# Optimization experiments

Measured on AMD Instinct MI355X. Metric: run time of the kernel, lower is better.

Reference implementation:

```python
import jax, jax.numpy as jnp
import numpy as np

N_VIEW = 100      # hardcoded n_view in _hard_anchor_sampling
TEMP = 20.0       # self.temperature
BASE_TEMP = 0.1   # self.base_temperature


def _sample_one(x, yh, yp, key):
    # x: [N, D] flattened spatial features, yh = labels, yp = predict (flattened)
    N = yh.shape[0]
    ar = jnp.arange(N)
    hard_mask = (yh == 0) & (yp == 0)            # (y_hat==0)&(y==0)
    easy_mask = (yh == 1) & (yp == 1)            # (y_hat==1)&(y==1)
    # torch keeps the first 50 hard nonzero indices (randperm over range(50) only permutes them)
    hard_idx = jnp.argsort(jnp.where(hard_mask, ar, N))[:N_VIEW // 2]
    # torch keeps a random 50-subset of the easy positives (randperm sampling)
    scores = jnp.where(easy_mask, jax.random.uniform(key, (N,)), -1.0)
    _, easy_idx = jax.lax.top_k(scores, N_VIEW // 2)
    # X_[ii, 0:50] = easy, X_[ii, 50:100] = hard
    return jnp.concatenate([x[easy_idx], x[hard_idx]], axis=0)  # [100, D]


def _contrastive(X_):
    # X_: [2, 100, D]; torch.cat(torch.unbind(X_, dim=1), dim=0) interleaves views-major
    A = jnp.swapaxes(X_, 0, 1).reshape(2 * N_VIEW, -1)  # [200, D]
    # F.normalize (contrast_feature is the same normalized anchor in the source)
    A = A / jnp.maximum(jnp.linalg.norm(A, axis=1, keepdims=True), 1e-12)
    logits = (A @ A.T) / BASE_TEMP
    logits = logits - jax.lax.stop_gradient(jnp.max(logits, axis=1, keepdims=True))
    idx = jnp.arange(2 * N_VIEW)
    # mask = kron([[1,0],[0,1]], ones(100,100)) -> 100x100 block diagonal
    mask0 = (idx[:, None] // N_VIEW == idx[None, :] // N_VIEW).astype(logits.dtype)
    neg_mask = 1.0 - mask0  # computed BEFORE logits_mask is applied
    # scatter_(1, arange(100).view(-1,1), 0) on a 200x200 tensor only zeros the
    # diagonal of the first 100 rows
    r = jnp.arange(N_VIEW)
    logits_mask = jnp.ones_like(mask0).at[r, r].set(0.0)
    mask = mask0 * logits_mask
    exp_l = jnp.exp(logits)
    neg = (exp_l * neg_mask).sum(axis=1, keepdims=True)
    log_prob = jnp.log(exp_l / (exp_l + neg))
    mean_lpp = (log_prob * mask).sum(axis=1) / mask.sum(axis=1)
    return -(mean_lpp / TEMP).mean()


def _forward(feats, labels, predict):
    B, D = feats.shape[0], feats.shape[1]
    x = jnp.moveaxis(feats, 1, -1).reshape(B, -1, D)  # [B, N, D]
    yh = labels.reshape(B, -1)
    yp = predict.reshape(B, -1)
    keys = jax.random.split(jax.random.key(42), B)
    X_ = jax.vmap(_sample_one)(x, yh, yp, keys)       # [2, 100, D]
    return _contrastive(X_)


def setup_inputs() -> dict:
    key = jax.random.key(0)
    k1, k2, k3 = jax.random.split(key, 3)
    feats = jax.random.normal(k1, (2, 128, 32, 64, 64), dtype=jnp.float32)
    labels = jax.random.randint(k2, (2, 32, 64, 64), 0, 2)
    predict = jax.random.randint(k3, (2, 32, 64, 64), 0, 2)
    return {"feats": feats, "labels": labels, "predict": predict}


def reference(feats, labels, predict):
    return _forward(feats, labels, predict)
```

## Files before the change

### kernel.cpp

```cpp
#include <hip/hip_runtime.h>
#include <stdint.h>

#define NPIX   131072
#define HALFN  65536
#define KSEL   50
#define CAP_E  1024
#define CAP_H  2048
#define THR    0.99f
#define CSTR   32
#define SENT_HARD 0xFFFFFFFFu
#define SENT_NONE 0xFFFFFFFEu

__host__ __device__ __forceinline__ uint32_t rotl32(uint32_t v, int d) {
  return (v << d) | (v >> (32 - d));
}

__host__ __device__ __forceinline__ void tf_block(uint32_t k0, uint32_t k1,
                                                  uint32_t c0, uint32_t c1,
                                                  uint32_t& o0, uint32_t& o1) {
  uint32_t ks2 = k0 ^ k1 ^ 0x1BD11BDAu;
  uint32_t x0 = c0 + k0, x1 = c1 + k1;
#define TF_R(r) { x0 += x1; x1 = rotl32(x1, (r)); x1 ^= x0; }
  TF_R(13) TF_R(15) TF_R(26) TF_R(6)   x0 += k1;  x1 += ks2 + 1u;
  TF_R(17) TF_R(29) TF_R(16) TF_R(24)  x0 += ks2; x1 += k0  + 2u;
  TF_R(13) TF_R(15) TF_R(26) TF_R(6)   x0 += k0;  x1 += k1  + 3u;
  TF_R(17) TF_R(29) TF_R(16) TF_R(24)  x0 += k1;  x1 += ks2 + 4u;
  TF_R(13) TF_R(15) TF_R(26) TF_R(6)   x0 += ks2; x1 += k0  + 5u;
#undef TF_R
  o0 = x0; o1 = x1;
}

__global__ void k_zero(int* cnts, float* out) {
  int i = threadIdx.x;
  if (i < 8 * CSTR) cnts[i] = 0;
  if (i == 0) out[0] = 0.f;
}

__global__ __launch_bounds__(512) void k_scores(
    const int* __restrict__ labels, const int* __restrict__ predict,
    uint32_t* __restrict__ scores, uint64_t* __restrict__ ecand,
    uint32_t* __restrict__ hcand, int* __restrict__ cnts,
    uint32_t k00, uint32_t k01, uint32_t k10, uint32_t k11) {
  int gid = blockIdx.x * blockDim.x + threadIdx.x;
  int b = gid >> 17;
  int n = gid & (NPIX - 1);
  int tid = threadIdx.x, wv = tid >> 6, lane = tid & 63;
  int yh = labels[gid], yp = predict[gid];
  bool is_easy = (yh == 1 && yp == 1);
  bool is_hard = (yh == 0 && yp == 0);
  uint32_t sval = SENT_NONE;
  float u = -1.f;
  if (is_easy) {
    uint32_t ka = b ? k10 : k00, kb = b ? k11 : k01;
    uint32_t o0, o1, bits;
    if (n < HALFN) { tf_block(ka, kb, (uint32_t)n, (uint32_t)(n + HALFN), o0, o1); bits = o0; }
    else           { tf_block(ka, kb, (uint32_t)(n - HALFN), (uint32_t)n, o0, o1); bits = o1; }
    u = __uint_as_float((bits >> 9) | 0x3F800000u) - 1.0f;
    sval = __float_as_uint(u);
  } else if (is_hard) {
    sval = SENT_HARD;
  }
  scores[gid] = sval;

  bool cand_e = is_easy && (u >= THR);
  bool cand_h = is_hard && (n < CAP_H);
  uint64_t bal_e  = __ballot(is_easy), bal_h  = __ballot(is_hard);
  uint64_t bal_ec = __ballot(cand_e),  bal_hc = __ballot(cand_h);

  __shared__ int we[8], wh[8], wec[8], whc[8];
  __shared__ int base_ec, base_hc;
  if (lane == 0) {
    we[wv]  = __popcll(bal_e);  wh[wv]  = __popcll(bal_h);
    wec[wv] = __popcll(bal_ec); whc[wv] = __popcll(bal_hc);
  }
  __syncthreads();
  if (tid == 0) {
    int te = 0, th = 0, tec = 0, thc = 0;
    for (int w = 0; w < 8; ++w) { te += we[w]; th += wh[w]; tec += wec[w]; thc += whc[w]; }
    if (te) atomicAdd(&cnts[(b * 4 + 0) * CSTR], te);
    if (th) atomicAdd(&cnts[(b * 4 + 2) * CSTR], th);
    base_ec = tec ? atomicAdd(&cnts[(b * 4 + 1) * CSTR], tec) : 0;
    base_hc = thc ? atomicAdd(&cnts[(b * 4 + 3) * CSTR], thc) : 0;
  }
  __syncthreads();
  if (cand_e) {
    int pre = 0;
    for (int w = 0; w < wv; ++w) pre += wec[w];
    int p = base_ec + pre + __popcll(bal_ec & ((1ull << lane) - 1));
    if (p < CAP_E)
      ecand[b * CAP_E + p] = ((uint64_t)sval << 32) | (uint32_t)(~(uint32_t)n);
  }
  if (cand_h) {
    int pre = 0;
    for (int w = 0; w < wv; ++w) pre += whc[w];
    int p = base_hc + pre + __popcll(bal_hc & ((1ull << lane) - 1));
    hcand[b * CAP_H + p] = (uint32_t)n;
  }
}

__device__ __forceinline__ bool cond_eval(uint32_t s, int cid) {
  return cid == 0 ? (s >= SENT_NONE) : (cid == 1 ? (s == SENT_HARD) : (s != SENT_HARD));
}

__device__ int nth_min_pred(const uint32_t* __restrict__ sc, int want, int cid,
                            int tid, int lane, int wv, uint32_t* s_w32, int* foundcnt) {
  int prev = -1;
  int k = 0;
  for (; k <= want; ++k) {
    uint32_t lmin = 0xFFFFFFFFu;
    for (int m = tid; m < NPIX; m += 128) {
      if (cond_eval(sc[m], cid) && m > prev && (uint32_t)m < lmin) lmin = (uint32_t)m;
    }
    for (int off = 32; off; off >>= 1) {
      uint32_t o = (uint32_t)__shfl_down(lmin, off);
      if (o < lmin) lmin = o;
    }
    if (lane == 0) s_w32[wv] = lmin;
    __syncthreads();
    uint32_t g = s_w32[0] < s_w32[1] ? s_w32[0] : s_w32[1];
    __syncthreads();
    if (g == 0xFFFFFFFFu) break;
    prev = (int)g;
  }
  *foundcnt = k;
  return prev;
}

__global__ __launch_bounds__(128) void k_selgather(
    const uint32_t* __restrict__ scores, const uint64_t* __restrict__ ecand,
    const uint32_t* __restrict__ hcand, const int* __restrict__ cnts,
    const float* __restrict__ feats, float* __restrict__ A) {
  int r = blockIdx.x;
  int tid = threadIdx.x;
  int lane = tid & 63, wv = tid >> 6;
  int v = r & 1, i = r >> 1;
  int b = v;
  const uint32_t* sc = scores + (size_t)b * NPIX;

  __shared__ uint64_t se[CAP_E];
  __shared__ uint32_t shd[CAP_H];
  __shared__ uint32_t s_w32[2];
  __shared__ uint64_t s_w64[2];
  __shared__ int s_n;

  int et = cnts[(b * 4 + 0) * CSTR], ec = cnts[(b * 4 + 1) * CSTR];
  int ht = cnts[(b * 4 + 2) * CSTR], hc = cnts[(b * 4 + 3) * CSTR];

  if (i < KSEL) {
    int eneed = et < KSEL ? et : KSEL;
    bool fast = (ec <= CAP_E) && (ec >= eneed);
    if (fast) {
      int take = ec < KSEL ? ec : KSEL;
      if (i < take) {
        for (int t = tid; t < ec; t += 128) se[t] = ecand[b * CAP_E + t];
        __syncthreads();
        for (int t = tid; t < ec; t += 128) {
          uint64_t mine = se[t];
          int rank = 0;
          for (int j = 0; j < ec; ++j) rank += (se[j] > mine);
          if (rank == i) s_n = (int)(~(uint32_t)mine);
        }
        __syncthreads();
      } else {
        int fc;
        int nsel = nth_min_pred(sc, i - take, 0, tid, lane, wv, s_w32, &fc);
        if (tid == 0) s_n = nsel;
        __syncthreads();
      }
    } else {
      uint64_t prev = 0xFFFFFFFFFFFFFFFFull;
      int found = 0, nsel = -1;
      for (int k = 0; k <= i; ++k) {
        uint64_t lmax = 0;
        for (int m = tid; m < NPIX; m += 128) {
          uint32_t s = sc[m];
          if (s < SENT_NONE) {
            uint64_t key = ((uint64_t)s << 32) | (uint32_t)(~(uint32_t)m);
            if (key < prev && key > lmax) lmax = key;
          }
        }
        for (int off = 32; off; off >>= 1) {
          uint64_t o = __shfl_down(lmax, off);
          if (o > lmax) lmax = o;
        }
        if (lane == 0) s_w64[wv] = lmax;
        __syncthreads();
        uint64_t g = s_w64[0] > s_w64[1] ? s_w64[0] : s_w64[1];
        __syncthreads();
        if (g == 0) break;
        prev = g; found = k + 1;
        if (k == i) nsel = (int)(~(uint32_t)g);
      }
      if (nsel < 0) {
        int fc;
        nsel = nth_min_pred(sc, i - found, 0, tid, lane, wv, s_w32, &fc);
      }
      if (tid == 0) s_n = nsel;
      __syncthreads();
    }
  } else {
    int j = i - KSEL;
    int hneed = ht < KSEL ? ht : KSEL;
    bool fast = (hc >= hneed);
    if (fast) {
      int take = hc < KSEL ? hc : KSEL;
      if (j < take) {
        for (int t = tid; t < hc; t += 128) shd[t] = hcand[b * CAP_H + t];
        __syncthreads();
        for (int t = tid; t < hc; t += 128) {
          uint32_t mine = shd[t];
          int rank = 0;
          for (int m = 0; m < hc; ++m) rank += (shd[m] < mine);
          if (rank == j) s_n = (int)mine;
        }
        __syncthreads();
      } else {
        int fc;
        int nsel = nth_min_pred(sc, j - take, 2, tid, lane, wv, s_w32, &fc);
        if (tid == 0) s_n = nsel;
        __syncthreads();
      }
    } else {
      int fc = 0;
      int nsel = nth_min_pred(sc, j, 1, tid, lane, wv, s_w32, &fc);
      if (fc < j + 1) {
        int fc2;
        nsel = nth_min_pred(sc, j - fc, 2, tid, lane, wv, s_w32, &fc2);
      }
      if (tid == 0) s_n = nsel;
      __syncthreads();
    }
  }

  int n = s_n;
  float val = feats[((size_t)(v * 128 + tid)) * NPIX + (size_t)n];
  float sq = val * val;
  for (int off = 32; off; off >>= 1) sq += __shfl_down(sq, off);
  __shared__ float wsum[2];
  __shared__ float s_inv;
  if (lane == 0) wsum[wv] = sq;
  __syncthreads();
  if (tid == 0) s_inv = 1.0f / fmaxf(sqrtf(wsum[0] + wsum[1]), 1e-12f);
  __syncthreads();
  A[r * 128 + tid] = val * s_inv;
}

__global__ __launch_bounds__(256) void k_loss(const float* __restrict__ A,
                                              float* __restrict__ out) {
  int r = blockIdx.x;
  int c = threadIdx.x;
  __shared__ float arow[128];
  __shared__ float red[256];
  if (c < 128) arow[c] = A[r * 128 + c];
  __syncthreads();
  bool valid = c < 200;
  float logit = -1e30f;
  if (valid) {
    const float* Ac = A + c * 128;
    float dot = 0.f;
#pragma unroll 8
    for (int d = 0; d < 128; ++d) dot += arow[d] * Ac[d];
    logit = dot * 10.0f;
  }
  red[c] = logit;
  __syncthreads();
  for (int s = 128; s; s >>= 1) { if (c < s) { float o = red[c + s]; if (o > red[c]) red[c] = o; } __syncthreads(); }
  float M = red[0];
  __syncthreads();
  float e = valid ? expf(logit - M) : 0.f;
  bool sameblk = valid && ((r / 100) == (c / 100));
  red[c] = (valid && !sameblk) ? e : 0.f;
  __syncthreads();
  for (int s = 128; s; s >>= 1) { if (c < s) red[c] += red[c + s]; __syncthreads(); }
  float neg = red[0];
  __syncthreads();
  bool msk = sameblk && !(r < 100 && c == r);
  red[c] = msk ? ((logit - M) - logf(e + neg)) : 0.f;
  __syncthreads();
  for (int s = 128; s; s >>= 1) { if (c < s) red[c] += red[c + s]; __syncthreads(); }
  if (c == 0) {
    float denom = (r < 100) ? 99.f : 100.f;
    atomicAdd(out, -(red[0] / denom) / (20.0f * 200.0f));
  }
}

extern "C" void kernel_launch(void* const* d_in, const int* in_sizes, int n_in,
                              void* d_out, int out_size, void* d_ws, size_t ws_size,
                              hipStream_t stream) {
  const float* feats  = (const float*)d_in[0];
  const int* labels   = (const int*)d_in[1];
  const int* predict  = (const int*)d_in[2];
  float* out = (float*)d_out;

  char* ws = (char*)d_ws;
  uint32_t* scores = (uint32_t*)ws;
  uint64_t* ecand  = (uint64_t*)(ws + (size_t)2 * NPIX * 4);
  uint32_t* hcand  = (uint32_t*)((char*)ecand + 2 * CAP_E * 8);
  int* cnts  = (int*)((char*)hcand + 2 * CAP_H * 4);
  float* A   = (float*)(cnts + 8 * CSTR);

  uint32_t a0, a1, b0, b1;
  tf_block(0u, 42u, 0u, 2u, a0, a1);
  tf_block(0u, 42u, 1u, 3u, b0, b1);

  k_zero<<<1, 256, 0, stream>>>(cnts, out);
  k_scores<<<(2 * NPIX) / 512, 512, 0, stream>>>(labels, predict, scores, ecand, hcand, cnts, a0, b0, a1, b1);
  k_selgather<<<200, 128, 0, stream>>>(scores, ecand, hcand, cnts, feats, A);
  k_loss<<<200, 256, 0, stream>>>(A, out);
}
```

Baseline: 202.5 us.

## Fuse all four kernels into one cooperative kernel with grid syncs

```diff
diff --git a/kernel.cpp b/kernel.cpp
--- a/kernel.cpp
+++ b/kernel.cpp
@@ -1,5 +1,8 @@
 #include <hip/hip_runtime.h>
+#include <hip/hip_cooperative_groups.h>
 #include <stdint.h>
+
+namespace cg = cooperative_groups;
 
 #define NPIX   131072
 #define HALFN  65536
@@ -10,6 +13,9 @@
 #define CSTR   32
 #define SENT_HARD 0xFFFFFFFFu
 #define SENT_NONE 0xFFFFFFFEu
+#define NBLK   256
+#define NTHR   512
+#define NWAVE  (NTHR / 64)
 
 __host__ __device__ __forceinline__ uint32_t rotl32(uint32_t v, int d) {
   return (v << d) | (v >> (32 - d));
@@ -30,74 +36,6 @@
   o0 = x0; o1 = x1;
 }
 
-__global__ void k_zero(int* cnts, float* out) {
-  int i = threadIdx.x;
-  if (i < 8 * CSTR) cnts[i] = 0;
-  if (i == 0) out[0] = 0.f;
-}
-
-__global__ __launch_bounds__(512) void k_scores(
-    const int* __restrict__ labels, const int* __restrict__ predict,
-    uint32_t* __restrict__ scores, uint64_t* __restrict__ ecand,
-    uint32_t* __restrict__ hcand, int* __restrict__ cnts,
-    uint32_t k00, uint32_t k01, uint32_t k10, uint32_t k11) {
-  int gid = blockIdx.x * blockDim.x + threadIdx.x;
-  int b = gid >> 17;
-  int n = gid & (NPIX - 1);
-  int tid = threadIdx.x, wv = tid >> 6, lane = tid & 63;
-  int yh = labels[gid], yp = predict[gid];
-  bool is_easy = (yh == 1 && yp == 1);
-  bool is_hard = (yh == 0 && yp == 0);
-  uint32_t sval = SENT_NONE;
-  float u = -1.f;
-  if (is_easy) {
-    uint32_t ka = b ? k10 : k00, kb = b ? k11 : k01;
-    uint32_t o0, o1, bits;
-    if (n < HALFN) { tf_block(ka, kb, (uint32_t)n, (uint32_t)(n + HALFN), o0, o1); bits = o0; }
-    else           { tf_block(ka, kb, (uint32_t)(n - HALFN), (uint32_t)n, o0, o1); bits = o1; }
-    u = __uint_as_float((bits >> 9) | 0x3F800000u) - 1.0f;
-    sval = __float_as_uint(u);
-  } else if (is_hard) {
-    sval = SENT_HARD;
-  }
-  scores[gid] = sval;
-
-  bool cand_e = is_easy && (u >= THR);
-  bool cand_h = is_hard && (n < CAP_H);
-  uint64_t bal_e  = __ballot(is_easy), bal_h  = __ballot(is_hard);
-  uint64_t bal_ec = __ballot(cand_e),  bal_hc = __ballot(cand_h);
-
-  __shared__ int we[8], wh[8], wec[8], whc[8];
-  __shared__ int base_ec, base_hc;
-  if (lane == 0) {
-    we[wv]  = __popcll(bal_e);  wh[wv]  = __popcll(bal_h);
-    wec[wv] = __popcll(bal_ec); whc[wv] = __popcll(bal_hc);
-  }
-  __syncthreads();
-  if (tid == 0) {
-    int te = 0, th = 0, tec = 0, thc = 0;
-    for (int w = 0; w < 8; ++w) { te += we[w]; th += wh[w]; tec += wec[w]; thc += whc[w]; }
-    if (te) atomicAdd(&cnts[(b * 4 + 0) * CSTR], te);
-    if (th) atomicAdd(&cnts[(b * 4 + 2) * CSTR], th);
-    base_ec = tec ? atomicAdd(&cnts[(b * 4 + 1) * CSTR], tec) : 0;
-    base_hc = thc ? atomicAdd(&cnts[(b * 4 + 3) * CSTR], thc) : 0;
-  }
-  __syncthreads();
-  if (cand_e) {
-    int pre = 0;
-    for (int w = 0; w < wv; ++w) pre += wec[w];
-    int p = base_ec + pre + __popcll(bal_ec & ((1ull << lane) - 1));
-    if (p < CAP_E)
-      ecand[b * CAP_E + p] = ((uint64_t)sval << 32) | (uint32_t)(~(uint32_t)n);
-  }
-  if (cand_h) {
-    int pre = 0;
-    for (int w = 0; w < wv; ++w) pre += whc[w];
-    int p = base_hc + pre + __popcll(bal_hc & ((1ull << lane) - 1));
-    hcand[b * CAP_H + p] = (uint32_t)n;
-  }
-}
-
 __device__ __forceinline__ bool cond_eval(uint32_t s, int cid) {
   return cid == 0 ? (s >= SENT_NONE) : (cid == 1 ? (s == SENT_HARD) : (s != SENT_HARD));
 }
@@ -108,7 +46,7 @@
   int k = 0;
   for (; k <= want; ++k) {
     uint32_t lmin = 0xFFFFFFFFu;
-    for (int m = tid; m < NPIX; m += 128) {
+    for (int m = tid; m < NPIX; m += NTHR) {
       if (cond_eval(sc[m], cid) && m > prev && (uint32_t)m < lmin) lmin = (uint32_t)m;
     }
     for (int off = 32; off; off >>= 1) {
@@ -117,7 +55,13 @@
     }
     if (lane == 0) s_w32[wv] = lmin;
     __syncthreads();
-    uint32_t g = s_w32[0] < s_w32[1] ? s_w32[0] : s_w32[1];
+    if (tid == 0) {
+      uint32_t g = 0xFFFFFFFFu;
+      for (int w = 0; w < NWAVE; ++w) if (s_w32[w] < g) g = s_w32[w];
+      s_w32[0] = g;
+    }
+    __syncthreads();
+    uint32_t g = s_w32[0];
     __syncthreads();
     if (g == 0xFFFFFFFFu) break;
     prev = (int)g;
@@ -126,161 +70,241 @@
   return prev;
 }
 
-__global__ __launch_bounds__(128) void k_selgather(
-    const uint32_t* __restrict__ scores, const uint64_t* __restrict__ ecand,
-    const uint32_t* __restrict__ hcand, const int* __restrict__ cnts,
-    const float* __restrict__ feats, float* __restrict__ A) {
-  int r = blockIdx.x;
-  int tid = threadIdx.x;
-  int lane = tid & 63, wv = tid >> 6;
-  int v = r & 1, i = r >> 1;
-  int b = v;
-  const uint32_t* sc = scores + (size_t)b * NPIX;
-
+__global__ __launch_bounds__(NTHR) void k_fused(
+    const int* __restrict__ labels, const int* __restrict__ predict,
+    const float* __restrict__ feats,
+    uint32_t* __restrict__ scores, uint64_t* __restrict__ ecand,
+    uint32_t* __restrict__ hcand, int* __restrict__ cnts,
+    float* __restrict__ A, float* __restrict__ out,
+    uint32_t k00, uint32_t k01, uint32_t k10, uint32_t k11) {
+  cg::grid_group grid = cg::this_grid();
+  int tid = threadIdx.x, lane = tid & 63, wv = tid >> 6;
+  int blk = blockIdx.x;
+
+  __shared__ int we[NWAVE], wh[NWAVE], wec[NWAVE], whc[NWAVE];
+  __shared__ int base_ec, base_hc;
   __shared__ uint64_t se[CAP_E];
   __shared__ uint32_t shd[CAP_H];
-  __shared__ uint32_t s_w32[2];
-  __shared__ uint64_t s_w64[2];
+  __shared__ uint32_t s_w32[NWAVE];
+  __shared__ uint64_t s_w64[NWAVE];
   __shared__ int s_n;
-
-  int et = cnts[(b * 4 + 0) * CSTR], ec = cnts[(b * 4 + 1) * CSTR];
-  int ht = cnts[(b * 4 + 2) * CSTR], hc = cnts[(b * 4 + 3) * CSTR];
-
-  if (i < KSEL) {
-    int eneed = et < KSEL ? et : KSEL;
-    bool fast = (ec <= CAP_E) && (ec >= eneed);
-    if (fast) {
-      int take = ec < KSEL ? ec : KSEL;
-      if (i < take) {
-        for (int t = tid; t < ec; t += 128) se[t] = ecand[b * CAP_E + t];
-        __syncthreads();
-        for (int t = tid; t < ec; t += 128) {
-          uint64_t mine = se[t];
-          int rank = 0;
-          for (int j = 0; j < ec; ++j) rank += (se[j] > mine);
-          if (rank == i) s_n = (int)(~(uint32_t)mine);
-        }
-        __syncthreads();
+  __shared__ float red[NTHR];
+  __shared__ float arow[128];
+  __shared__ float wsum[2];
+  __shared__ float s_inv;
+
+  if (blk == 0) {
+    if (tid < 8 * CSTR) cnts[tid] = 0;
+    if (tid == 0) out[0] = 0.f;
+  }
+  grid.sync();
+
+  for (int c = 0; c < 2; ++c) {
+    int gid = blk * (2 * NTHR) + c * NTHR + tid;
+    int b = gid >> 17;
+    int n = gid & (NPIX - 1);
+    int yh = labels[gid], yp = predict[gid];
+    bool is_easy = (yh == 1 && yp == 1);
+    bool is_hard = (yh == 0 && yp == 0);
+    uint32_t sval = SENT_NONE;
+    float u = -1.f;
+    if (is_easy) {
+      uint32_t ka = b ? k10 : k00, kb = b ? k11 : k01;
+      uint32_t o0, o1, bits;
+      if (n < HALFN) { tf_block(ka, kb, (uint32_t)n, (uint32_t)(n + HALFN), o0, o1); bits = o0; }
+      else           { tf_block(ka, kb, (uint32_t)(n - HALFN), (uint32_t)n, o0, o1); bits = o1; }
+      u = __uint_as_float((bits >> 9) | 0x3F800000u) - 1.0f;
+      sval = __float_as_uint(u);
+    } else if (is_hard) {
+      sval = SENT_HARD;
+    }
+    scores[gid] = sval;
+
+    bool cand_e = is_easy && (u >= THR);
+    bool cand_h = is_hard && (n < CAP_H);
+    uint64_t bal_e  = __ballot(is_easy), bal_h  = __ballot(is_hard);
+    uint64_t bal_ec = __ballot(cand_e),  bal_hc = __ballot(cand_h);
+
+    if (lane == 0) {
+      we[wv]  = __popcll(bal_e);  wh[wv]  = __popcll(bal_h);
+      wec[wv] = __popcll(bal_ec); whc[wv] = __popcll(bal_hc);
+    }
+    __syncthreads();
+    if (tid == 0) {
+      int te = 0, th = 0, tec = 0, thc = 0;
+      for (int w = 0; w < NWAVE; ++w) { te += we[w]; th += wh[w]; tec += wec[w]; thc += whc[w]; }
+      if (te) atomicAdd(&cnts[(b * 4 + 0) * CSTR], te);
+      if (th) atomicAdd(&cnts[(b * 4 + 2) * CSTR], th);
+      base_ec = tec ? atomicAdd(&cnts[(b * 4 + 1) * CSTR], tec) : 0;
+      base_hc = thc ? atomicAdd(&cnts[(b * 4 + 3) * CSTR], thc) : 0;
+    }
+    __syncthreads();
+    if (cand_e) {
+      int pre = 0;
+      for (int w = 0; w < wv; ++w) pre += wec[w];
+      int p = base_ec + pre + __popcll(bal_ec & ((1ull << lane) - 1));
+      if (p < CAP_E)
+        ecand[b * CAP_E + p] = ((uint64_t)sval << 32) | (uint32_t)(~(uint32_t)n);
+    }
+    if (cand_h) {
+      int pre = 0;
+      for (int w = 0; w < wv; ++w) pre += whc[w];
+      int p = base_hc + pre + __popcll(bal_hc & ((1ull << lane) - 1));
+      hcand[b * CAP_H + p] = (uint32_t)n;
+    }
+    __syncthreads();
+  }
+  grid.sync();
+
+  if (blk < 200) {
+    int r = blk;
+    int v = r & 1, i = r >> 1;
+    int b = v;
+    const uint32_t* sc = scores + (size_t)b * NPIX;
+
+    int et = cnts[(b * 4 + 0) * CSTR], ec = cnts[(b * 4 + 1) * CSTR];
+    int ht = cnts[(b * 4 + 2) * CSTR], hc = cnts[(b * 4 + 3) * CSTR];
+
+    if (i < KSEL) {
+      int eneed = et < KSEL ? et : KSEL;
+      bool fast = (ec <= CAP_E) && (ec >= eneed);
+      if (fast) {
+        int take = ec < KSEL ? ec : KSEL;
+        if (i < take) {
+          for (int t = tid; t < ec; t += NTHR) se[t] = ecand[b * CAP_E + t];
+          __syncthreads();
+          for (int t = tid; t < ec; t += NTHR) {
+            uint64_t mine = se[t];
+            int rank = 0;
+            for (int j = 0; j < ec; ++j) rank += (se[j] > mine);
+            if (rank == i) s_n = (int)(~(uint32_t)mine);
+          }
+          __syncthreads();
+        } else {
+          int fc;
+          int nsel = nth_min_pred(sc, i - take, 0, tid, lane, wv, s_w32, &fc);
+          if (tid == 0) s_n = nsel;
+          __syncthreads();
+        }
       } else {
-        int fc;
-        int nsel = nth_min_pred(sc, i - take, 0, tid, lane, wv, s_w32, &fc);
+        uint64_t prev = 0xFFFFFFFFFFFFFFFFull;
+        int found = 0, nsel = -1;
+        for (int k = 0; k <= i; ++k) {
+          uint64_t lmax = 0;
+          for (int m = tid; m < NPIX; m += NTHR) {
+            uint32_t s = sc[m];
+            if (s < SENT_NONE) {
+              uint64_t key = ((uint64_t)s << 32) | (uint32_t)(~(uint32_t)m);
+              if (key < prev && key > lmax) lmax = key;
+            }
+          }
+          for (int off = 32; off; off >>= 1) {
+            uint64_t o = __shfl_down(lmax, off);
+            if (o > lmax) lmax = o;
+          }
+          if (lane == 0) s_w64[wv] = lmax;
+          __syncthreads();
+          if (tid == 0) {
+            uint64_t g = 0;
+            for (int w = 0; w < NWAVE; ++w) if (s_w64[w] > g) g = s_w64[w];
+            s_w64[0] = g;
+          }
+          __syncthreads();
+          uint64_t g = s_w64[0];
+          __syncthreads();
+          if (g == 0) break;
+          prev = g; found = k + 1;
+          if (k == i) nsel = (int)(~(uint32_t)g);
+        }
+        if (nsel < 0) {
+          int fc;
+          nsel = nth_min_pred(sc, i - found, 0, tid, lane, wv, s_w32, &fc);
+        }
         if (tid == 0) s_n = nsel;
         __syncthreads();
       }
     } else {
-      uint64_t prev = 0xFFFFFFFFFFFFFFFFull;
-      int found = 0, nsel = -1;
-      for (int k = 0; k <= i; ++k) {
-        uint64_t lmax = 0;
-        for (int m = tid; m < NPIX; m += 128) {
-          uint32_t s = sc[m];
-          if (s < SENT_NONE) {
-            uint64_t key = ((uint64_t)s << 32) | (uint32_t)(~(uint32_t)m);
-            if (key < prev && key > lmax) lmax = key;
-          }
-        }
-        for (int off = 32; off; off >>= 1) {
-          uint64_t o = __shfl_down(lmax, off);
-          if (o > lmax) lmax = o;
-        }
-        if (lane == 0) s_w64[wv] = lmax;
-        __syncthreads();
-        uint64_t g = s_w64[0] > s_w64[1] ? s_w64[0] : s_w64[1];
-        __syncthreads();
-        if (g == 0) break;
-        prev = g; found = k + 1;
-        if (k == i) nsel = (int)(~(uint32_t)g);
-      }
-      if (nsel < 0) {
-        int fc;
-        nsel = nth_min_pred(sc, i - found, 0, tid, lane, wv, s_w32, &fc);
-      }
-      if (tid == 0) s_n = nsel;
-      __syncthreads();
-    }
-  } else {
-    int j = i - KSEL;
-    int hneed = ht < KSEL ? ht : KSEL;
-    bool fast = (hc >= hneed);
-    if (fast) {
-      int take = hc < KSEL ? hc : KSEL;
-      if (j < take) {
-        for (int t = tid; t < hc; t += 128) shd[t] = hcand[b * CAP_H + t];
-        __syncthreads();
-        for (int t = tid; t < hc; t += 128) {
-          uint32_t mine = shd[t];
-          int rank = 0;
-          for (int m = 0; m < hc; ++m) rank += (shd[m] < mine);
-          if (rank == j) s_n = (int)mine;
-        }
-        __syncthreads();
+      int j = i - KSEL;
+      int hneed = ht < KSEL ? ht : KSEL;
+      bool fast = (hc >= hneed);
+      if (fast) {
+        int take = hc < KSEL ? hc : KSEL;
+        if (j < take) {
+          for (int t = tid; t < hc; t += NTHR) shd[t] = hcand[b * CAP_H + t];
+          __syncthreads();
+          for (int t = tid; t < hc; t += NTHR) {
+            uint32_t mine = shd[t];
+            int rank = 0;
+            for (int m = 0; m < hc; ++m) rank += (shd[m] < mine);
+            if (rank == j) s_n = (int)mine;
+          }
+          __syncthreads();
+        } else {
+          int fc;
+          int nsel = nth_min_pred(sc, j - take, 2, tid, lane, wv, s_w32, &fc);
+          if (tid == 0) s_n = nsel;
+          __syncthreads();
+        }
       } else {
-        int fc;
-        int nsel = nth_min_pred(sc, j - take, 2, tid, lane, wv, s_w32, &fc);
+        int fc = 0;
+        int nsel = nth_min_pred(sc, j, 1, tid, lane, wv, s_w32, &fc);
+        if (fc < j + 1) {
+          int fc2;
+          nsel = nth_min_pred(sc, j - fc, 2, tid, lane, wv, s_w32, &fc2);
+        }
         if (tid == 0) s_n = nsel;
         __syncthreads();
       }
-    } else {
-      int fc = 0;
-      int nsel = nth_min_pred(sc, j, 1, tid, lane, wv, s_w32, &fc);
-      if (fc < j + 1) {
-        int fc2;
-        nsel = nth_min_pred(sc, j - fc, 2, tid, lane, wv, s_w32, &fc2);
-      }
-      if (tid == 0) s_n = nsel;
-      __syncthreads();
-    }
-  }
-
-  int n = s_n;
-  float val = feats[((size_t)(v * 128 + tid)) * NPIX + (size_t)n];
-  float sq = val * val;
-  for (int off = 32; off; off >>= 1) sq += __shfl_down(sq, off);
-  __shared__ float wsum[2];
-  __shared__ float s_inv;
-  if (lane == 0) wsum[wv] = sq;
-  __syncthreads();
-  if (tid == 0) s_inv = 1.0f / fmaxf(sqrtf(wsum[0] + wsum[1]), 1e-12f);
-  __syncthreads();
-  A[r * 128 + tid] = val * s_inv;
-}
-
-__global__ __launch_bounds__(256) void k_loss(const float* __restrict__ A,
-                                              float* __restrict__ out) {
-  int r = blockIdx.x;
-  int c = threadIdx.x;
-  __shared__ float arow[128];
-  __shared__ float red[256];
-  if (c < 128) arow[c] = A[r * 128 + c];
-  __syncthreads();
-  bool valid = c < 200;
-  float logit = -1e30f;
-  if (valid) {
-    const float* Ac = A + c * 128;
-    float dot = 0.f;
+    }
+
+    int n = s_n;
+    if (tid < 128) {
+      float val = feats[((size_t)(v * 128 + tid)) * NPIX + (size_t)n];
+      float sq = val * val;
+      for (int off = 32; off; off >>= 1) sq += __shfl_down(sq, off);
+      if (lane == 0) wsum[wv] = sq;
+      red[tid] = val;
+    }
+    __syncthreads();
+    if (tid == 0) s_inv = 1.0f / fmaxf(sqrtf(wsum[0] + wsum[1]), 1e-12f);
+    __syncthreads();
+    if (tid < 128) A[r * 128 + tid] = red[tid] * s_inv;
+  }
+  grid.sync();
+
+  if (blk < 200) {
+    int r = blk;
+    if (tid < 128) arow[tid] = A[r * 128 + tid];
+    __syncthreads();
+    bool valid = tid < 200;
+    float logit = -1e30f;
+    if (valid) {
+      const float* Ac = A + tid * 128;
+      float dot = 0.f;
 #pragma unroll 8
-    for (int d = 0; d < 128; ++d) dot += arow[d] * Ac[d];
-    logit = dot * 10.0f;
-  }
-  red[c] = logit;
-  __syncthreads();
-  for (int s = 128; s; s >>= 1) { if (c < s) { float o = red[c + s]; if (o > red[c]) red[c] = o; } __syncthreads(); }
-  float M = red[0];
-  __syncthreads();
-  float e = valid ? expf(logit - M) : 0.f;
-  bool sameblk = valid && ((r / 100) == (c / 100));
-  red[c] = (valid && !sameblk) ? e : 0.f;
-  __syncthreads();
-  for (int s = 128; s; s >>= 1) { if (c < s) red[c] += red[c + s]; __syncthreads(); }
-  float neg = red[0];
-  __syncthreads();
-  bool msk = sameblk && !(r < 100 && c == r);
-  red[c] = msk ? ((logit - M) - logf(e + neg)) : 0.f;
-  __syncthreads();
-  for (int s = 128; s; s >>= 1) { if (c < s) red[c] += red[c + s]; __syncthreads(); }
-  if (c == 0) {
-    float denom = (r < 100) ? 99.f : 100.f;
-    atomicAdd(out, -(red[0] / denom) / (20.0f * 200.0f));
+      for (int d = 0; d < 128; ++d) dot += arow[d] * Ac[d];
+      logit = dot * 10.0f;
+    }
+    red[tid] = logit;
+    __syncthreads();
+    for (int s = NTHR / 2; s; s >>= 1) { if (tid < s) { float o = red[tid + s]; if (o > red[tid]) red[tid] = o; } __syncthreads(); }
+    float M = red[0];
+    __syncthreads();
+    float e = valid ? expf(logit - M) : 0.f;
+    bool sameblk = valid && ((r / 100) == (tid / 100));
+    red[tid] = (valid && !sameblk) ? e : 0.f;
+    __syncthreads();
+    for (int s = NTHR / 2; s; s >>= 1) { if (tid < s) red[tid] += red[tid + s]; __syncthreads(); }
+    float neg = red[0];
+    __syncthreads();
+    bool msk = sameblk && !(r < 100 && tid == r);
+    red[tid] = msk ? ((logit - M) - logf(e + neg)) : 0.f;
+    __syncthreads();
+    for (int s = NTHR / 2; s; s >>= 1) { if (tid < s) red[tid] += red[tid + s]; __syncthreads(); }
+    if (tid == 0) {
+      float denom = (r < 100) ? 99.f : 100.f;
+      atomicAdd(out, -(red[0] / denom) / (20.0f * 200.0f));
+    }
   }
 }
 
@@ -303,8 +327,9 @@
   tf_block(0u, 42u, 0u, 2u, a0, a1);
   tf_block(0u, 42u, 1u, 3u, b0, b1);
 
-  k_zero<<<1, 256, 0, stream>>>(cnts, out);
-  k_scores<<<(2 * NPIX) / 512, 512, 0, stream>>>(labels, predict, scores, ecand, hcand, cnts, a0, b0, a1, b1);
-  k_selgather<<<200, 128, 0, stream>>>(scores, ecand, hcand, cnts, feats, A);
-  k_loss<<<200, 256, 0, stream>>>(A, out);
-}
+  void* args[] = {(void*)&labels, (void*)&predict, (void*)&feats,
+                  (void*)&scores, (void*)&ecand, (void*)&hcand, (void*)&cnts,
+                  (void*)&A, (void*)&out,
+                  (void*)&a0, (void*)&b0, (void*)&a1, (void*)&b1};
+  hipLaunchCooperativeKernel((void*)k_fused, dim3(NBLK), dim3(NTHR), args, 0, stream);
+}
```

Measured after the change: 264.3 us. +30.5%, slower.
